# Kernel tuning notes

Measured on AMD Instinct MI355X. Metric: run time of the kernel, lower is better.

The kernel has to match this reference:

```python
import jax, jax.numpy as jnp
import numpy as np
from jax import lax

EPS = 1e-5
T, N, E = 10, 10000, 320000
C_IN, C_HID, C_OUT = 16, 32, 16


def _stgcn_layer(x, edge_index, edge_weight, tw, tb, gw, gb, gamma, beta):
    # x: [T, N, Cin] -> temporal conv over T per node
    xc = jnp.transpose(x, (1, 2, 0))  # [N, Cin, T]
    y = lax.conv_general_dilated(xc, tw, window_strides=(1,), padding=((1, 1),),
                                 dimension_numbers=("NCH", "OIH", "NCH"))
    y = y + tb[None, :, None]
    y = jnp.clip(y, -10.0, 10.0)
    # InstanceNorm1d (affine, biased var over time axis)
    mu = jnp.mean(y, axis=-1, keepdims=True)
    var = jnp.mean((y - mu) ** 2, axis=-1, keepdims=True)
    y = (y - mu) * lax.rsqrt(var + EPS) * gamma[None, :, None] + beta[None, :, None]
    y = jax.nn.relu(y)
    h = jnp.transpose(y, (0, 2, 1))  # [N, T, C]

    n = h.shape[0]
    # GCNConv normalization (identical at every timestep -> computed once)
    ewn = jax.nn.softmax(edge_weight)  # softmax over all E edges
    loop = jnp.arange(n, dtype=edge_index.dtype)
    row = jnp.concatenate([edge_index[0], loop])  # sources (+self loops)
    col = jnp.concatenate([edge_index[1], loop])  # destinations
    w = jnp.concatenate([ewn, jnp.ones((n,), dtype=ewn.dtype)])
    deg = jax.ops.segment_sum(w, col, num_segments=n)
    dinv = jnp.where(deg > 0, lax.rsqrt(jnp.maximum(deg, EPS * 0 + 1e-30)), 0.0)
    norm = dinv[row] * w * dinv[col]  # [E+N]

    hw = jnp.einsum("ntc,cd->ntd", h, gw)  # [N, T, C]
    msg = hw[row] * norm[:, None, None]     # [E+N, T, C] gather
    agg = jax.ops.segment_sum(msg, col, num_segments=n) + gb  # scatter-add
    out = jnp.clip(jax.nn.relu(agg), -10.0, 10.0)
    return jnp.transpose(out, (1, 0, 2))  # [T, N, C]


def setup_inputs() -> dict:
    key = jax.random.key(0)
    ks = jax.random.split(key, 16)
    inp = {
        "x": jax.random.normal(ks[0], (T, N, C_IN), dtype=jnp.float32),
        "edge_index": jax.random.randint(ks[1], (2, E), 0, N, dtype=jnp.int32),
        "edge_weight": jax.random.uniform(ks[2], (E,), dtype=jnp.float32),
        # layer 1 (in -> hid)
        "l1_tw": jax.random.normal(ks[3], (C_HID, C_IN, 3), dtype=jnp.float32) * 0.02,
        "l1_tb": jnp.zeros((C_HID,), dtype=jnp.float32),
        "l1_gw": jax.random.normal(ks[4], (C_HID, C_HID), dtype=jnp.float32) * 0.1,
        "l1_gb": jnp.zeros((C_HID,), dtype=jnp.float32),
        "l1_gamma": jnp.ones((C_HID,), dtype=jnp.float32),
        "l1_beta": jnp.zeros((C_HID,), dtype=jnp.float32),
        # layer 2 (hid -> hid)
        "l2_tw": jax.random.normal(ks[5], (C_HID, C_HID, 3), dtype=jnp.float32) * 0.02,
        "l2_tb": jnp.zeros((C_HID,), dtype=jnp.float32),
        "l2_gw": jax.random.normal(ks[6], (C_HID, C_HID), dtype=jnp.float32) * 0.1,
        "l2_gb": jnp.zeros((C_HID,), dtype=jnp.float32),
        "l2_gamma": jnp.ones((C_HID,), dtype=jnp.float32),
        "l2_beta": jnp.zeros((C_HID,), dtype=jnp.float32),
        # output linear
        "out_w": jax.random.normal(ks[7], (C_HID, C_OUT), dtype=jnp.float32) * 0.1,
        "out_b": jnp.zeros((C_OUT,), dtype=jnp.float32),
    }
    return inp


def reference(x, edge_index, edge_weight,
              l1_tw, l1_tb, l1_gw, l1_gb, l1_gamma, l1_beta,
              l2_tw, l2_tb, l2_gw, l2_gb, l2_gamma, l2_beta,
              out_w, out_b):
    h = _stgcn_layer(x, edge_index, edge_weight, l1_tw, l1_tb, l1_gw, l1_gb, l1_gamma, l1_beta)
    h = _stgcn_layer(h, edge_index, edge_weight, l2_tw, l2_tb, l2_gw, l2_gb, l2_gamma, l2_beta)
    # per-timestep linear then mean over time == mean then linear, done faithfully
    outs = jnp.einsum("tnc,cd->tnd", h, out_w) + out_b
    return jnp.mean(outs, axis=0)  # [N, C_OUT]
```

## Files before the change

kernel.cpp:

```cpp
#include <hip/hip_runtime.h>
#include <hip/hip_bf16.h>
#include <string.h>


typedef __hip_bfloat16 bf16;

#define TSTEPS 10
#define TPAD 12
#define CHID 32
#define ROWELE (TSTEPS * CHID)

__device__ __forceinline__ float b2f(bf16 v) { return __bfloat162float(v); }
__device__ __forceinline__ float ldf(const void* p, long i, int bf) {
    return bf ? __bfloat162float(((const bf16*)p)[i]) : ((const float*)p)[i];
}
__device__ __forceinline__ int detect_bf(const unsigned* gbits) {
    return (gbits[0] != 0x3F800000u) ? 1 : 0;
}
__device__ __forceinline__ float bflo(unsigned u) { return __uint_as_float(u << 16); }
__device__ __forceinline__ float bfhi(unsigned u) { return __uint_as_float(u & 0xFFFF0000u); }
__device__ __forceinline__ unsigned pack2bf(float a, float b) {
    bf16 x = __float2bfloat16(a), y = __float2bfloat16(b);
    unsigned short ux, uy;
    memcpy(&ux, &x, 2); memcpy(&uy, &y, 2);
    return (unsigned)ux | ((unsigned)uy << 16);
}


__global__ __launch_bounds__(256) void edge_pass_kernel(
    const void* __restrict__ ew, const unsigned* __restrict__ gbits,
    const int* __restrict__ ei,
    float* __restrict__ ewn, float* __restrict__ degx, int* __restrict__ cnt,
    float* sumexp, int E) {
    int bf = detect_bf(gbits);
    int i = blockIdx.x * 256 + threadIdx.x;
    float e = 0.0f;
    if (i < E) {
        float w = ldf(ew, i, bf);
        e = __expf(w);
        ewn[i] = e;
        int c = ei[E + i];
        atomicAdd(&degx[c], e);
        atomicAdd(&cnt[c], 1);
    }
    float v = e;
    for (int o = 32; o > 0; o >>= 1) v += __shfl_down(v, o);
    __shared__ float s[4];
    int lane = threadIdx.x & 63, wv = threadIdx.x >> 6;
    if (lane == 0) s[wv] = v;
    __syncthreads();
    if (threadIdx.x == 0) atomicAdd(sumexp, s[0] + s[1] + s[2] + s[3]);
}

__global__ __launch_bounds__(1024) void scan_kernel(const int* __restrict__ cnt,
                                                    const float* __restrict__ degx,
                                                    const float* __restrict__ sumexp,
                                                    float* __restrict__ dinv,
                                                    int* __restrict__ off, int N) {
    __shared__ int s[1024];
    int tid = threadIdx.x;
    float invS = 1.0f / (*sumexp);
    for (int i = tid; i < N; i += 1024) dinv[i] = rsqrtf(1.0f + degx[i] * invS);
    int chunk = (N + 1023) / 1024;
    int b0 = tid * chunk;
    int p = 0;
    for (int k = 0; k < chunk; k++) { int i = b0 + k; if (i < N) p += cnt[i]; }
    s[tid] = p;
    __syncthreads();
    for (int d = 1; d < 1024; d <<= 1) {
        int v = (tid >= d) ? s[tid - d] : 0;
        __syncthreads();
        s[tid] += v;
        __syncthreads();
    }
    int base = s[tid] - p;
    for (int k = 0; k < chunk; k++) {
        int i = b0 + k;
        if (i < N) {
            off[i] = base;
            base += cnt[i];
            if (i == N - 1) off[N] = base;
        }
    }
}

__global__ __launch_bounds__(256) void fill_kernel(const int* __restrict__ ei,
                                                   const float* __restrict__ ewn,
                                                   const float* __restrict__ dinv,
                                                   const float* __restrict__ sumexp,
                                                   const int* __restrict__ off,
                                                   int* __restrict__ cursor,
                                                   int* __restrict__ csr_src,
                                                   float* __restrict__ csr_w, int E) {
    int i = blockIdx.x * 256 + threadIdx.x;
    if (i >= E) return;
    float invS = 1.0f / (*sumexp);
    int r = ei[i], c = ei[E + i];
    int p = atomicAdd(&cursor[c], 1);
    int idx = off[c] + p;
    csr_src[idx] = r;
    csr_w[idx] = dinv[r] * (ewn[i] * invS) * dinv[c];
}


template <int CIN, int LAYOUT>
__global__ __launch_bounds__(256) void conv_kernel(
    const void* __restrict__ in_, const unsigned* __restrict__ gbits,
    const void* __restrict__ tw, const void* __restrict__ tb,
    const void* __restrict__ gamma, const void* __restrict__ beta,
    const void* __restrict__ gw,
    bf16* __restrict__ hw, int N) {
    constexpr int CO = CHID;
    __shared__ __align__(16) float s_in[8 * CIN * TPAD];
    __shared__ __align__(16) float s_h[8 * CO * TPAD];
    __shared__ float s_tw[3 * CIN * CO];
    __shared__ float s_gw[CO * CO];
    __shared__ float s_tb[CO], s_ga[CO], s_be[CO];

    int bfw = detect_bf(gbits);
    int tid = threadIdx.x;
    for (int i = tid; i < CO * CIN * 3; i += 256) {
        int o = i / (CIN * 3);
        int rem = i % (CIN * 3);
        int ci = rem / 3, k = rem % 3;
        s_tw[(k * CIN + ci) * CO + o] = ldf(tw, i, bfw);
    }
    for (int i = tid; i < CO * CO; i += 256) s_gw[i] = ldf(gw, i, bfw);
    if (tid < CO) {
        s_tb[tid] = ldf(tb, tid, bfw);
        s_ga[tid] = ldf(gamma, tid, bfw);
        s_be[tid] = ldf(beta, tid, bfw);
    }

    int nb = blockIdx.x * 8;

    if (LAYOUT == 0) {
        constexpr int CP = CIN / 2;
        for (int i2 = tid; i2 < 8 * TSTEPS * CP; i2 += 256) {
            int cp = i2 % CP;
            int t = (i2 / CP) % TSTEPS;
            int nl = i2 / (CP * TSTEPS);
            int n = nb + nl;
            float v0 = 0.0f, v1 = 0.0f;
            if (n < N) {
                long idx = (long)t * ((long)N * CIN) + (long)n * CIN + 2 * cp;
                if (bfw) {
                    unsigned u = ((const unsigned*)in_)[idx >> 1];
                    v0 = bflo(u); v1 = bfhi(u);
                } else {
                    float2 f = ((const float2*)in_)[idx >> 1];
                    v0 = f.x; v1 = f.y;
                }
            }
            int b = nl * (CIN * TPAD) + (2 * cp) * TPAD + t;
            s_in[b] = v0;
            s_in[b + TPAD] = v1;
        }
    } else {
        for (int i2 = tid; i2 < 8 * CIN * 5; i2 += 256) {
            int tp = i2 % 5;
            int ci = (i2 / 5) % CIN;
            int nl = i2 / (5 * CIN);
            int n = nb + nl;
            float v0 = 0.0f, v1 = 0.0f;
            if (n < N) {
                long idx = (long)n * (CIN * TSTEPS) + ci * TSTEPS + 2 * tp;
                unsigned u = ((const unsigned*)in_)[idx >> 1];
                v0 = bflo(u); v1 = bfhi(u);
            }
            int b = nl * (CIN * TPAD) + ci * TPAD + 2 * tp;
            s_in[b] = v0;
            s_in[b + 1] = v1;
        }
    }
    __syncthreads();

    int nl = tid >> 5, o = tid & 31;
    int n = nb + nl;
    const float* xrow = &s_in[nl * CIN * TPAD];

    float acc[TSTEPS];
    float tbv = s_tb[o];
#pragma unroll
    for (int t = 0; t < TSTEPS; t++) acc[t] = tbv;

    for (int ci = 0; ci < CIN; ci++) {
        const float4* xp = (const float4*)&xrow[ci * TPAD];
        float4 A = xp[0], B = xp[1], C = xp[2];
        float xr[TSTEPS] = {A.x, A.y, A.z, A.w, B.x, B.y, B.z, B.w, C.x, C.y};
        float w0 = s_tw[(0 * CIN + ci) * CO + o];
        float w1 = s_tw[(1 * CIN + ci) * CO + o];
        float w2 = s_tw[(2 * CIN + ci) * CO + o];
        acc[0] += xr[0] * w1 + xr[1] * w2;
#pragma unroll
        for (int t = 1; t < TSTEPS - 1; t++)
            acc[t] += xr[t - 1] * w0 + xr[t] * w1 + xr[t + 1] * w2;
        acc[TSTEPS - 1] += xr[TSTEPS - 2] * w0 + xr[TSTEPS - 1] * w1;
    }

#pragma unroll
    for (int t = 0; t < TSTEPS; t++) acc[t] = fminf(fmaxf(acc[t], -10.0f), 10.0f);
    float mu = 0.0f;
#pragma unroll
    for (int t = 0; t < TSTEPS; t++) mu += acc[t];
    mu *= 0.1f;
    float var = 0.0f;
#pragma unroll
    for (int t = 0; t < TSTEPS; t++) { float d = acc[t] - mu; var += d * d; }
    var *= 0.1f;
    float sc = s_ga[o] * rsqrtf(var + 1e-5f);
    float be = s_be[o];
    float h[TSTEPS];
#pragma unroll
    for (int t = 0; t < TSTEPS; t++) h[t] = fmaxf((acc[t] - mu) * sc + be, 0.0f);

    float4* hp = (float4*)&s_h[nl * CO * TPAD + o * TPAD];
    hp[0] = make_float4(h[0], h[1], h[2], h[3]);
    hp[1] = make_float4(h[4], h[5], h[6], h[7]);
    hp[2] = make_float4(h[8], h[9], 0.0f, 0.0f);
    __syncthreads();

    float acc2[TSTEPS];
#pragma unroll
    for (int t = 0; t < TSTEPS; t++) acc2[t] = 0.0f;
    const float* hrow = &s_h[nl * CO * TPAD];
    for (int c = 0; c < CO; c++) {
        const float4* cp4 = (const float4*)&hrow[c * TPAD];
        float4 A = cp4[0], B = cp4[1], C = cp4[2];
        float g = s_gw[c * CO + o];
        acc2[0] += A.x * g; acc2[1] += A.y * g; acc2[2] += A.z * g; acc2[3] += A.w * g;
        acc2[4] += B.x * g; acc2[5] += B.y * g; acc2[6] += B.z * g; acc2[7] += B.w * g;
        acc2[8] += C.x * g; acc2[9] += C.y * g;
    }
    if (n < N) {
        unsigned* hwp = (unsigned*)hw;
        long base = (long)n * (ROWELE / 2) + o * (TSTEPS / 2);
#pragma unroll
        for (int j = 0; j < 5; j++)
            hwp[base + j] = pack2bf(acc2[2 * j], acc2[2 * j + 1]);
    }
}


__global__ __launch_bounds__(ROWELE) void agg_kernel(
    const bf16* __restrict__ hw, const int* __restrict__ off,
    const int* __restrict__ csr_src, const float* __restrict__ csr_w,
    const float* __restrict__ dinv, const void* __restrict__ gb,
    const unsigned* __restrict__ gbits,
    bf16* __restrict__ out, int N) {
    __shared__ int s_src[ROWELE];
    __shared__ float s_w[ROWELE];
    int bf = detect_bf(gbits);
    int n = blockIdx.x;
    int tid = threadIdx.x;
    float dn = dinv[n];
    float acc = b2f(hw[(long)n * ROWELE + tid]) * (dn * dn);
    int beg = off[n], end = off[n + 1];
    for (int base = beg; base < end; base += ROWELE) {
        int m = min(ROWELE, end - base);
        if (tid < m) { s_src[tid] = csr_src[base + tid]; s_w[tid] = csr_w[base + tid]; }
        __syncthreads();
        int j = 0;
        for (; j + 4 <= m; j += 4) {
            int r0 = s_src[j], r1 = s_src[j + 1], r2 = s_src[j + 2], r3 = s_src[j + 3];
            float w0 = s_w[j], w1 = s_w[j + 1], w2 = s_w[j + 2], w3 = s_w[j + 3];
            acc += b2f(hw[(long)r0 * ROWELE + tid]) * w0;
            acc += b2f(hw[(long)r1 * ROWELE + tid]) * w1;
            acc += b2f(hw[(long)r2 * ROWELE + tid]) * w2;
            acc += b2f(hw[(long)r3 * ROWELE + tid]) * w3;
        }
        for (; j < m; j++) acc += b2f(hw[(long)s_src[j] * ROWELE + tid]) * s_w[j];
        __syncthreads();
    }
    int c = tid / TSTEPS;
    float v = acc + ldf(gb, c, bf);
    v = fminf(fmaxf(v, 0.0f), 10.0f);
    out[(long)n * ROWELE + tid] = __float2bfloat16(v);
}


__global__ __launch_bounds__(ROWELE) void agg_final_kernel(
    const bf16* __restrict__ hw, const int* __restrict__ off,
    const int* __restrict__ csr_src, const float* __restrict__ csr_w,
    const float* __restrict__ dinv, const void* __restrict__ gb,
    const void* __restrict__ ow, const void* __restrict__ ob,
    const unsigned* __restrict__ gbits,
    void* __restrict__ out, int N) {
    __shared__ int s_src[ROWELE];
    __shared__ float s_w[ROWELE];
    __shared__ float s_row[ROWELE];
    __shared__ float s_hbar[CHID];
    __shared__ float s_ow[CHID * 16];
    __shared__ float s_ob[16];
    int bf = detect_bf(gbits);
    int n = blockIdx.x;
    int tid = threadIdx.x;
    for (int i = tid; i < CHID * 16; i += ROWELE) s_ow[i] = ldf(ow, i, bf);
    if (tid < 16) s_ob[tid] = ldf(ob, tid, bf);

    float dn = dinv[n];
    float acc = b2f(hw[(long)n * ROWELE + tid]) * (dn * dn);
    int beg = off[n], end = off[n + 1];
    for (int base = beg; base < end; base += ROWELE) {
        int m = min(ROWELE, end - base);
        if (tid < m) { s_src[tid] = csr_src[base + tid]; s_w[tid] = csr_w[base + tid]; }
        __syncthreads();
        int j = 0;
        for (; j + 4 <= m; j += 4) {
            int r0 = s_src[j], r1 = s_src[j + 1], r2 = s_src[j + 2], r3 = s_src[j + 3];
            float w0 = s_w[j], w1 = s_w[j + 1], w2 = s_w[j + 2], w3 = s_w[j + 3];
            acc += b2f(hw[(long)r0 * ROWELE + tid]) * w0;
            acc += b2f(hw[(long)r1 * ROWELE + tid]) * w1;
            acc += b2f(hw[(long)r2 * ROWELE + tid]) * w2;
            acc += b2f(hw[(long)r3 * ROWELE + tid]) * w3;
        }
        for (; j < m; j++) acc += b2f(hw[(long)s_src[j] * ROWELE + tid]) * s_w[j];
        __syncthreads();
    }
    int c = tid / TSTEPS;
    float v = acc + ldf(gb, c, bf);
    v = fminf(fmaxf(v, 0.0f), 10.0f);
    s_row[tid] = v;
    __syncthreads();
    if (tid < CHID) {
        float s = 0.0f;
#pragma unroll
        for (int t = 0; t < TSTEPS; t++) s += s_row[tid * TSTEPS + t];
        s_hbar[tid] = s * 0.1f;
    }
    __syncthreads();
    if (tid < 16) {
        float a = s_ob[tid];
#pragma unroll
        for (int cc = 0; cc < CHID; cc++) a += s_hbar[cc] * s_ow[cc * 16 + tid];
        long oi = (long)n * 16 + tid;
        if (bf) ((bf16*)out)[oi] = __float2bfloat16(a);
        else    ((float*)out)[oi] = a;
    }
}


extern "C" void kernel_launch(void* const* d_in, const int* in_sizes, int n_in,
                              void* d_out, int out_size, void* d_ws, size_t ws_size,
                              hipStream_t stream) {
    (void)n_in; (void)out_size; (void)ws_size;

    const void* x     = d_in[0];
    const int*  ei    = (const int*)d_in[1];
    const void* ew    = d_in[2];
    const void* l1_tw = d_in[3];
    const void* l1_tb = d_in[4];
    const void* l1_gw = d_in[5];
    const void* l1_gb = d_in[6];
    const unsigned* gbits = (const unsigned*)d_in[7];
    const void* l1_ga = d_in[7];
    const void* l1_be = d_in[8];
    const void* l2_tw = d_in[9];
    const void* l2_tb = d_in[10];
    const void* l2_gw = d_in[11];
    const void* l2_gb = d_in[12];
    const void* l2_ga = d_in[13];
    const void* l2_be = d_in[14];
    const void* out_w = d_in[15];
    const void* out_b = d_in[16];

    const int N = in_sizes[0] / (TSTEPS * 16);
    const int E = in_sizes[1] / 2;

    char* p = (char*)d_ws;
    auto alloc = [&](size_t bytes) -> char* {
        char* r = p;
        p += (bytes + 255) & ~(size_t)255;
        return r;
    };
    char* zbase   = p;
    float* sumexp = (float*)alloc(256);
    float* degx   = (float*)alloc((size_t)N * 4);
    int*   cnt    = (int*)alloc((size_t)N * 4);
    int*   cursor = (int*)alloc((size_t)N * 4);
    size_t zbytes = (size_t)(p - zbase);
    float* ewn     = (float*)alloc((size_t)E * 4);
    float* dinv    = (float*)alloc((size_t)N * 4);
    int*   offA    = (int*)alloc((size_t)(N + 1) * 4);
    int*   csr_src = (int*)alloc((size_t)E * 4);
    float* csr_w   = (float*)alloc((size_t)E * 4);
    bf16*  bufA    = (bf16*)alloc((size_t)N * ROWELE * 2);
    bf16*  bufB    = (bf16*)alloc((size_t)N * ROWELE * 2);

    int gE = (E + 255) / 256;
    int gConv = (N + 7) / 8;

    hipMemsetAsync(zbase, 0, zbytes, stream);
    hipLaunchKernelGGL(edge_pass_kernel, dim3(gE), dim3(256), 0, stream,
                       ew, gbits, ei, ewn, degx, cnt, sumexp, E);
    hipLaunchKernelGGL(scan_kernel, dim3(1), dim3(1024), 0, stream,
                       cnt, degx, sumexp, dinv, offA, N);
    hipLaunchKernelGGL(fill_kernel, dim3(gE), dim3(256), 0, stream,
                       ei, ewn, dinv, sumexp, offA, cursor, csr_src, csr_w, E);

    hipLaunchKernelGGL((conv_kernel<16, 0>), dim3(gConv), dim3(256), 0, stream,
                       x, gbits, l1_tw, l1_tb, l1_ga, l1_be, l1_gw, bufA, N);
    hipLaunchKernelGGL(agg_kernel, dim3(N), dim3(ROWELE), 0, stream,
                       bufA, offA, csr_src, csr_w, dinv, l1_gb, gbits, bufB, N);
    hipLaunchKernelGGL((conv_kernel<32, 1>), dim3(gConv), dim3(256), 0, stream,
                       (const void*)bufB, gbits, l2_tw, l2_tb, l2_ga, l2_be, l2_gw, bufA, N);
    hipLaunchKernelGGL(agg_final_kernel, dim3(N), dim3(ROWELE), 0, stream,
                       bufA, offA, csr_src, csr_w, dinv, l2_gb, out_w, out_b, gbits,
                       d_out, N);
}
```

Measured before the change: 315.1 us.

## Vectorize aggregation gathers to 16-byte loads and split edges across thread groups

The aggregation kernels now have each thread load a uint4 (8 bf16 values) of a neighbor row instead of one bf16. The 320 threads split into 8 edge-groups of 40 lanes, each group handling every 8th edge, and the 8 partial sums are reduced through shared memory. This is meant to cut the number of load instructions and raise memory-level parallelism in the gather, which dominates runtime. The cost is extra shared-memory traffic and syncs for the reduction, plus wasted lanes when a node has few edges.

```diff
diff --git a/kernel.cpp b/kernel.cpp
--- a/kernel.cpp
+++ b/kernel.cpp
@@ -9,6 +9,7 @@
 #define TPAD 12
 #define CHID 32
 #define ROWELE (TSTEPS * CHID)
+#define ROWW4 40
 
 __device__ __forceinline__ float b2f(bf16 v) { return __bfloat162float(v); }
 __device__ __forceinline__ float ldf(const void* p, long i, int bf) {
@@ -24,6 +25,12 @@
     unsigned short ux, uy;
     memcpy(&ux, &x, 2); memcpy(&uy, &y, 2);
     return (unsigned)ux | ((unsigned)uy << 16);
+}
+__device__ __forceinline__ void accum8(float* f, uint4 u, float w) {
+    f[0] += w * bflo(u.x); f[1] += w * bfhi(u.x);
+    f[2] += w * bflo(u.y); f[3] += w * bfhi(u.y);
+    f[4] += w * bflo(u.z); f[5] += w * bfhi(u.z);
+    f[6] += w * bflo(u.w); f[7] += w * bfhi(u.w);
 }
 
 
@@ -242,45 +249,9 @@
 }
 
 
-__global__ __launch_bounds__(ROWELE) void agg_kernel(
-    const bf16* __restrict__ hw, const int* __restrict__ off,
-    const int* __restrict__ csr_src, const float* __restrict__ csr_w,
-    const float* __restrict__ dinv, const void* __restrict__ gb,
-    const unsigned* __restrict__ gbits,
-    bf16* __restrict__ out, int N) {
-    __shared__ int s_src[ROWELE];
-    __shared__ float s_w[ROWELE];
-    int bf = detect_bf(gbits);
-    int n = blockIdx.x;
-    int tid = threadIdx.x;
-    float dn = dinv[n];
-    float acc = b2f(hw[(long)n * ROWELE + tid]) * (dn * dn);
-    int beg = off[n], end = off[n + 1];
-    for (int base = beg; base < end; base += ROWELE) {
-        int m = min(ROWELE, end - base);
-        if (tid < m) { s_src[tid] = csr_src[base + tid]; s_w[tid] = csr_w[base + tid]; }
-        __syncthreads();
-        int j = 0;
-        for (; j + 4 <= m; j += 4) {
-            int r0 = s_src[j], r1 = s_src[j + 1], r2 = s_src[j + 2], r3 = s_src[j + 3];
-            float w0 = s_w[j], w1 = s_w[j + 1], w2 = s_w[j + 2], w3 = s_w[j + 3];
-            acc += b2f(hw[(long)r0 * ROWELE + tid]) * w0;
-            acc += b2f(hw[(long)r1 * ROWELE + tid]) * w1;
-            acc += b2f(hw[(long)r2 * ROWELE + tid]) * w2;
-            acc += b2f(hw[(long)r3 * ROWELE + tid]) * w3;
-        }
-        for (; j < m; j++) acc += b2f(hw[(long)s_src[j] * ROWELE + tid]) * s_w[j];
-        __syncthreads();
-    }
-    int c = tid / TSTEPS;
-    float v = acc + ldf(gb, c, bf);
-    v = fminf(fmaxf(v, 0.0f), 10.0f);
-    out[(long)n * ROWELE + tid] = __float2bfloat16(v);
-}
-
-
-__global__ __launch_bounds__(ROWELE) void agg_final_kernel(
-    const bf16* __restrict__ hw, const int* __restrict__ off,
+template <bool FINAL>
+__global__ __launch_bounds__(320) void agg_kernel_t(
+    const uint4* __restrict__ hw4, const int* __restrict__ off,
     const int* __restrict__ csr_src, const float* __restrict__ csr_w,
     const float* __restrict__ dinv, const void* __restrict__ gb,
     const void* __restrict__ ow, const void* __restrict__ ob,
@@ -288,54 +259,96 @@
     void* __restrict__ out, int N) {
     __shared__ int s_src[ROWELE];
     __shared__ float s_w[ROWELE];
-    __shared__ float s_row[ROWELE];
+    __shared__ float s_part[8 * ROWW4 * 9];
     __shared__ float s_hbar[CHID];
     __shared__ float s_ow[CHID * 16];
     __shared__ float s_ob[16];
+
     int bf = detect_bf(gbits);
     int n = blockIdx.x;
     int tid = threadIdx.x;
-    for (int i = tid; i < CHID * 16; i += ROWELE) s_ow[i] = ldf(ow, i, bf);
-    if (tid < 16) s_ob[tid] = ldf(ob, tid, bf);
+    int g = tid % ROWW4;
+    int eo = tid / ROWW4;
+
+    if (FINAL) {
+        for (int i = tid; i < CHID * 16; i += ROWELE) s_ow[i] = ldf(ow, i, bf);
+        if (tid < 16) s_ob[tid] = ldf(ob, tid, bf);
+    }
+
+    float facc[8];
+#pragma unroll
+    for (int j = 0; j < 8; j++) facc[j] = 0.0f;
 
     float dn = dinv[n];
-    float acc = b2f(hw[(long)n * ROWELE + tid]) * (dn * dn);
+    if (eo == 0) {
+        uint4 u = hw4[n * ROWW4 + g];
+        accum8(facc, u, dn * dn);
+    }
+
     int beg = off[n], end = off[n + 1];
     for (int base = beg; base < end; base += ROWELE) {
         int m = min(ROWELE, end - base);
         if (tid < m) { s_src[tid] = csr_src[base + tid]; s_w[tid] = csr_w[base + tid]; }
         __syncthreads();
-        int j = 0;
-        for (; j + 4 <= m; j += 4) {
-            int r0 = s_src[j], r1 = s_src[j + 1], r2 = s_src[j + 2], r3 = s_src[j + 3];
-            float w0 = s_w[j], w1 = s_w[j + 1], w2 = s_w[j + 2], w3 = s_w[j + 3];
-            acc += b2f(hw[(long)r0 * ROWELE + tid]) * w0;
-            acc += b2f(hw[(long)r1 * ROWELE + tid]) * w1;
-            acc += b2f(hw[(long)r2 * ROWELE + tid]) * w2;
-            acc += b2f(hw[(long)r3 * ROWELE + tid]) * w3;
-        }
-        for (; j < m; j++) acc += b2f(hw[(long)s_src[j] * ROWELE + tid]) * s_w[j];
-        __syncthreads();
-    }
+        int kmax = (m + 7) >> 3;
+        int k = 0;
+        for (; k + 2 <= kmax; k += 2) {
+            int j0 = (k << 3) + eo, j1 = j0 + 8;
+            int c0 = min(j0, m - 1), c1 = min(j1, m - 1);
+            float w0 = (j0 < m) ? s_w[c0] : 0.0f;
+            float w1 = (j1 < m) ? s_w[c1] : 0.0f;
+            int r0 = s_src[c0], r1 = s_src[c1];
+            uint4 u0 = hw4[r0 * ROWW4 + g];
+            uint4 u1 = hw4[r1 * ROWW4 + g];
+            accum8(facc, u0, w0);
+            accum8(facc, u1, w1);
+        }
+        if (k < kmax) {
+            int j0 = (k << 3) + eo;
+            int c0 = min(j0, m - 1);
+            float w0 = (j0 < m) ? s_w[c0] : 0.0f;
+            int r0 = s_src[c0];
+            uint4 u0 = hw4[r0 * ROWW4 + g];
+            accum8(facc, u0, w0);
+        }
+        __syncthreads();
+    }
+
+    {
+        float* rowp = &s_part[(eo * ROWW4 + g) * 9];
+#pragma unroll
+        for (int j = 0; j < 8; j++) rowp[j] = facc[j];
+    }
+    __syncthreads();
+    int gg = tid >> 3, jj = tid & 7;
+    float v = 0.0f;
+#pragma unroll
+    for (int s = 0; s < 8; s++) v += s_part[(s * ROWW4 + gg) * 9 + jj];
     int c = tid / TSTEPS;
-    float v = acc + ldf(gb, c, bf);
+    v += ldf(gb, c, bf);
     v = fminf(fmaxf(v, 0.0f), 10.0f);
-    s_row[tid] = v;
-    __syncthreads();
-    if (tid < CHID) {
-        float s = 0.0f;
-#pragma unroll
-        for (int t = 0; t < TSTEPS; t++) s += s_row[tid * TSTEPS + t];
-        s_hbar[tid] = s * 0.1f;
-    }
-    __syncthreads();
-    if (tid < 16) {
-        float a = s_ob[tid];
-#pragma unroll
-        for (int cc = 0; cc < CHID; cc++) a += s_hbar[cc] * s_ow[cc * 16 + tid];
-        long oi = (long)n * 16 + tid;
-        if (bf) ((bf16*)out)[oi] = __float2bfloat16(a);
-        else    ((float*)out)[oi] = a;
+
+    if (!FINAL) {
+        ((bf16*)out)[(long)n * ROWELE + tid] = __float2bfloat16(v);
+    } else {
+        __syncthreads();
+        s_part[tid] = v;
+        __syncthreads();
+        if (tid < CHID) {
+            float s = 0.0f;
+#pragma unroll
+            for (int t = 0; t < TSTEPS; t++) s += s_part[tid * TSTEPS + t];
+            s_hbar[tid] = s * 0.1f;
+        }
+        __syncthreads();
+        if (tid < 16) {
+            float a = s_ob[tid];
+#pragma unroll
+            for (int cc = 0; cc < CHID; cc++) a += s_hbar[cc] * s_ow[cc * 16 + tid];
+            long oi = (long)n * 16 + tid;
+            if (bf) ((bf16*)out)[oi] = __float2bfloat16(a);
+            else    ((float*)out)[oi] = a;
+        }
     }
 }
 
@@ -400,11 +413,12 @@
 
     hipLaunchKernelGGL((conv_kernel<16, 0>), dim3(gConv), dim3(256), 0, stream,
                        x, gbits, l1_tw, l1_tb, l1_ga, l1_be, l1_gw, bufA, N);
-    hipLaunchKernelGGL(agg_kernel, dim3(N), dim3(ROWELE), 0, stream,
-                       bufA, offA, csr_src, csr_w, dinv, l1_gb, gbits, bufB, N);
+    hipLaunchKernelGGL((agg_kernel_t<false>), dim3(N), dim3(ROWELE), 0, stream,
+                       (const uint4*)bufA, offA, csr_src, csr_w, dinv, l1_gb,
+                       nullptr, nullptr, gbits, (void*)bufB, N);
     hipLaunchKernelGGL((conv_kernel<32, 1>), dim3(gConv), dim3(256), 0, stream,
                        (const void*)bufB, gbits, l2_tw, l2_tb, l2_ga, l2_be, l2_gw, bufA, N);
-    hipLaunchKernelGGL(agg_final_kernel, dim3(N), dim3(ROWELE), 0, stream,
-                       bufA, offA, csr_src, csr_w, dinv, l2_gb, out_w, out_b, gbits,
-                       d_out, N);
-}
+    hipLaunchKernelGGL((agg_kernel_t<true>), dim3(N), dim3(ROWELE), 0, stream,
+                       (const uint4*)bufA, offA, csr_src, csr_w, dinv, l2_gb,
+                       out_w, out_b, gbits, d_out, N);
+}
```

Result: faster. 287.4 us (-8.8%).
